# Optimization experiments

Measured on AMD Instinct MI355X. Metric: run time of the kernel, lower is better.

The kernel has to match this reference:

```python
import jax, jax.numpy as jnp
import numpy as np

N_NODES = 50000
N_EDGES = 800000
IN_CH = 64
HID = 64
N_LAYERS = 4


def setup_inputs() -> dict:
    key = jax.random.key(0)
    ks = jax.random.split(key, 10)
    x = jax.random.normal(ks[0], (N_NODES, IN_CH), dtype=jnp.float32)
    edge_index = jax.random.randint(ks[1], (2, N_EDGES), 0, N_NODES, dtype=jnp.int32)
    # SAGEConv params per layer: lin_l (applied to aggregated neighbors, with bias)
    # and lin_r (applied to root node). All layers are 64->64 so stack to [L, in, out].
    s = 1.0 / np.sqrt(IN_CH)
    Wl = jax.random.uniform(ks[2], (N_LAYERS, IN_CH, HID), jnp.float32, -s, s)
    Wr = jax.random.uniform(ks[3], (N_LAYERS, IN_CH, HID), jnp.float32, -s, s)
    b = jax.random.uniform(ks[4], (N_LAYERS, HID), jnp.float32, -s, s)
    alpha = jnp.full((N_LAYERS, HID), 0.25, dtype=jnp.float32)  # PReLU init
    return {"x": x, "edge_index": edge_index, "Wl": Wl, "Wr": Wr, "b": b, "alpha": alpha}


def _sage_layer(x, src, dst, deg_inv, Wl, Wr, b):
    # mean aggregation of source-node features at destination nodes
    agg = jax.ops.segment_sum(x[src], dst, num_segments=N_NODES)  # [N, d]
    agg = agg * deg_inv[:, None]
    return agg @ Wl + x @ Wr + b


def _prelu(x, a):
    return jnp.where(x >= 0, x, a * x)


def reference(x, edge_index, Wl, Wr, b, alpha):
    src, dst = edge_index[0], edge_index[1]
    deg = jax.ops.segment_sum(jnp.ones((N_EDGES,), jnp.float32), dst, num_segments=N_NODES)
    deg_inv = 1.0 / jnp.maximum(deg, 1.0)
    for i in range(N_LAYERS):
        x = _sage_layer(x, src, dst, deg_inv, Wl[i], Wr[i], b[i])
        x = _prelu(x, alpha[i])
    return x
```

## Files before the change

### kernel.cpp

```cpp
#include <hip/hip_runtime.h>

#define NN 50000
#define NE 800000
#define C 64
#define NL 4
#define NBK 196
#define HBLK 782

typedef __attribute__((ext_vector_type(8))) short bf16x8;
typedef __attribute__((ext_vector_type(4))) float f32x4;

__device__ __forceinline__ unsigned short f2bf(float f) {
    unsigned u = __float_as_uint(f);
    u += 0x7fffu + ((u >> 16) & 1u);
    return (unsigned short)(u >> 16);
}
__device__ __forceinline__ float4 bf4_to_f4(uint2 p) {
    float4 r;
    r.x = __uint_as_float(p.x << 16);
    r.y = __uint_as_float(p.x & 0xffff0000u);
    r.z = __uint_as_float(p.y << 16);
    r.w = __uint_as_float(p.y & 0xffff0000u);
    return r;
}

__global__ __launch_bounds__(1024) void bucket_hist_kernel(const int* __restrict__ dst,
                                                           int* __restrict__ blk_cnt,
                                                           int* __restrict__ lrank) {
    __shared__ int cnt[NBK];
    int tid = threadIdx.x;
    int blk = blockIdx.x;
    if (tid < NBK) cnt[tid] = 0;
    __syncthreads();
    int e = blk * 1024 + tid;
    if (e < NE) lrank[e] = atomicAdd(&cnt[dst[e] >> 8], 1);
    __syncthreads();
    if (tid < NBK) blk_cnt[tid * HBLK + blk] = cnt[tid];
}

__global__ __launch_bounds__(1024) void scanblk_kernel(int* __restrict__ blk_cnt,
                                                       int* __restrict__ bucket_tot) {
    __shared__ int sdata[1024];
    int b = blockIdx.x;
    int tid = threadIdx.x;
    int v = (tid < HBLK) ? blk_cnt[b * HBLK + tid] : 0;
    sdata[tid] = v;
    __syncthreads();
    for (int off = 1; off < 1024; off <<= 1) {
        int t = (tid >= off) ? sdata[tid - off] : 0;
        __syncthreads();
        sdata[tid] += t;
        __syncthreads();
    }
    if (tid < HBLK) blk_cnt[b * HBLK + tid] = sdata[tid] - v;
    if (tid == HBLK - 1) bucket_tot[b] = sdata[tid];
}

__global__ __launch_bounds__(1024) void bucket_scatter_kernel(
    const int* __restrict__ src, const int* __restrict__ dst,
    const int* __restrict__ lrank, const int* __restrict__ base2,
    const int* __restrict__ bucket_tot, int2* __restrict__ sorted) {
    __shared__ int sscan[256];
    __shared__ int sex[256];
    int tid = threadIdx.x;
    int blk = blockIdx.x;
    int v0 = 0;
    if (tid < 256) {
        v0 = (tid < NBK) ? bucket_tot[tid] : 0;
        sscan[tid] = v0;
    }
    __syncthreads();
    for (int off = 1; off < 256; off <<= 1) {
        int t = (tid < 256 && tid >= off) ? sscan[tid - off] : 0;
        __syncthreads();
        if (tid < 256) sscan[tid] += t;
        __syncthreads();
    }
    if (tid < 256) sex[tid] = sscan[tid] - v0;
    __syncthreads();

    int e = blk * 1024 + tid;
    if (e < NE) {
        int d = dst[e];
        int b = d >> 8;
        int pos = sex[b] + base2[b * HBLK + blk] + lrank[e];
        sorted[pos] = make_int2(src[e], d);
    }
}

__global__ __launch_bounds__(512) void bucket_finalize_kernel(
    const int2* __restrict__ sorted, const int* __restrict__ bucket_tot,
    int* __restrict__ row_start, int* __restrict__ deg, float* __restrict__ deg_inv,
    int* __restrict__ csr_src) {
    __shared__ int sscan[256];
    __shared__ int ldeg[256];
    __shared__ int lpre[256];
    __shared__ int lcnt[256];

    int b = blockIdx.x;
    int tid = threadIdx.x;
    int v0 = 0;
    if (tid < 256) {
        v0 = (tid < NBK) ? bucket_tot[tid] : 0;
        sscan[tid] = v0;
        ldeg[tid] = 0;
        lcnt[tid] = 0;
    }
    __syncthreads();
    for (int off = 1; off < 256; off <<= 1) {
        int t = (tid < 256 && tid >= off) ? sscan[tid - off] : 0;
        __syncthreads();
        if (tid < 256) sscan[tid] += t;
        __syncthreads();
    }
    int lo = (b == 0) ? 0 : sscan[b - 1];
    int hi = sscan[b];
    __syncthreads();

    for (int i = lo + tid; i < hi; i += 512)
        atomicAdd(&ldeg[sorted[i].y & 255], 1);
    __syncthreads();

    int dv = 0;
    if (tid < 256) {
        dv = ldeg[tid];
        lpre[tid] = dv;
    }
    __syncthreads();
    for (int off = 1; off < 256; off <<= 1) {
        int t = (tid < 256 && tid >= off) ? lpre[tid - off] : 0;
        __syncthreads();
        if (tid < 256) lpre[tid] += t;
        __syncthreads();
    }
    if (tid < 256) {
        int p = lpre[tid] - dv;
        lpre[tid] = p;
        int n = b * 256 + tid;
        if (n < NN) {
            row_start[n] = lo + p;
            deg[n] = dv;
            deg_inv[n] = 1.0f / fmaxf((float)dv, 1.0f);
        }
    }
    __syncthreads();

    for (int i = lo + tid; i < hi; i += 512) {
        int2 p = sorted[i];
        int loc = p.y & 255;
        int r = atomicAdd(&lcnt[loc], 1);
        csr_src[lo + lpre[loc] + r] = p.x;
    }
}

__global__ __launch_bounds__(512) void transform_mfma_kernel(
    const float* __restrict__ xin,
    const float* __restrict__ Wl, const float* __restrict__ Wr,
    const float* __restrict__ bias,
    unsigned short* __restrict__ y, float* __restrict__ z)
{
    __shared__ unsigned short xs[64][72];
    __shared__ unsigned short wlT[64][72];
    __shared__ unsigned short wrT[64][72];
    __shared__ unsigned short ys[64][64];
    __shared__ float zs[64][64];
    __shared__ float bs[C];

    int tid = threadIdx.x;
    int node0 = blockIdx.x * 64;

    for (int i = tid; i < C * C; i += 512) {
        int k = i >> 6, c = i & 63;
        wlT[c][k] = f2bf(Wl[i]);
        wrT[c][k] = f2bf(Wr[i]);
    }
    if (tid < C) bs[tid] = bias[tid];
    for (int i = tid; i < 64 * 16; i += 512) {
        int nl = i >> 4, c4 = i & 15;
        int n = node0 + nl;
        int nc = n < NN ? n : NN - 1;
        float4 v = ((const float4*)xin)[(size_t)nc * 16 + c4];
        xs[nl][c4 * 4 + 0] = f2bf(v.x);
        xs[nl][c4 * 4 + 1] = f2bf(v.y);
        xs[nl][c4 * 4 + 2] = f2bf(v.z);
        xs[nl][c4 * 4 + 3] = f2bf(v.w);
    }
    __syncthreads();

    int w = tid >> 6;
    int l = tid & 63;
    int mt = w >> 1;
    int half = w & 1;
    int r16 = l & 15;
    int kg = l >> 4;

    bf16x8 a0 = *(const bf16x8*)&xs[mt * 16 + r16][kg * 8];
    bf16x8 a1 = *(const bf16x8*)&xs[mt * 16 + r16][32 + kg * 8];

    f32x4 acc[4];
    #pragma unroll
    for (int nt = 0; nt < 4; nt++) {
        float bv = half ? bs[nt * 16 + r16] : 0.f;
        acc[nt] = (f32x4){bv, bv, bv, bv};
    }
    #pragma unroll
    for (int nt = 0; nt < 4; nt++) {
        const unsigned short* col = half ? &wrT[nt * 16 + r16][0] : &wlT[nt * 16 + r16][0];
        bf16x8 b0 = *(const bf16x8*)&col[kg * 8];
        bf16x8 b1 = *(const bf16x8*)&col[32 + kg * 8];
        acc[nt] = __builtin_amdgcn_mfma_f32_16x16x32_bf16(a0, b0, acc[nt], 0, 0, 0);
        acc[nt] = __builtin_amdgcn_mfma_f32_16x16x32_bf16(a1, b1, acc[nt], 0, 0, 0);
    }
    #pragma unroll
    for (int nt = 0; nt < 4; nt++) {
        #pragma unroll
        for (int j = 0; j < 4; j++) {
            int r = mt * 16 + kg * 4 + j;
            int c = nt * 16 + r16;
            if (half) zs[r][c] = acc[nt][j];
            else      ys[r][c] = f2bf(acc[nt][j]);
        }
    }
    __syncthreads();

    for (int i = tid; i < 64 * 16; i += 512) {
        int r = i >> 4, g = i & 15;
        int n = node0 + r;
        if (n < NN) {
            ((ushort4*)&y[(size_t)n * C])[g] = ((const ushort4*)&ys[r][0])[g];
            ((float4*)&z[(size_t)n * C])[g] = ((const float4*)&zs[r][0])[g];
        }
    }
}

__device__ __forceinline__ float4 gather_row(const uint2* __restrict__ yb,
                                             const int* __restrict__ cp, int d, int ql) {
    float4 acc = make_float4(0.f, 0.f, 0.f, 0.f);
    for (int t = 0; t < d; t += 8) {
        int lim = d - 1 - t;
        int j1 = min(1, lim), j2 = min(2, lim), j3 = min(3, lim);
        int j4 = min(4, lim), j5 = min(5, lim), j6 = min(6, lim), j7 = min(7, lim);
        float m1 = lim >= 1 ? 1.f : 0.f, m2 = lim >= 2 ? 1.f : 0.f;
        float m3 = lim >= 3 ? 1.f : 0.f, m4 = lim >= 4 ? 1.f : 0.f;
        float m5 = lim >= 5 ? 1.f : 0.f, m6 = lim >= 6 ? 1.f : 0.f;
        float m7 = lim >= 7 ? 1.f : 0.f;
        int s0 = cp[t];
        int s1 = cp[t + j1];
        int s2 = cp[t + j2];
        int s3 = cp[t + j3];
        int s4 = cp[t + j4];
        int s5 = cp[t + j5];
        int s6 = cp[t + j6];
        int s7 = cp[t + j7];
        uint2 p0 = yb[(size_t)s0 * 16 + ql];
        uint2 p1 = yb[(size_t)s1 * 16 + ql];
        uint2 p2 = yb[(size_t)s2 * 16 + ql];
        uint2 p3 = yb[(size_t)s3 * 16 + ql];
        uint2 p4 = yb[(size_t)s4 * 16 + ql];
        uint2 p5 = yb[(size_t)s5 * 16 + ql];
        uint2 p6 = yb[(size_t)s6 * 16 + ql];
        uint2 p7 = yb[(size_t)s7 * 16 + ql];
        float4 v0 = bf4_to_f4(p0);
        float4 v1 = bf4_to_f4(p1);
        float4 v2 = bf4_to_f4(p2);
        float4 v3 = bf4_to_f4(p3);
        float4 v4 = bf4_to_f4(p4);
        float4 v5 = bf4_to_f4(p5);
        float4 v6 = bf4_to_f4(p6);
        float4 v7 = bf4_to_f4(p7);
        acc.x += v0.x;      acc.y += v0.y;      acc.z += v0.z;      acc.w += v0.w;
        acc.x += v1.x * m1; acc.y += v1.y * m1; acc.z += v1.z * m1; acc.w += v1.w * m1;
        acc.x += v2.x * m2; acc.y += v2.y * m2; acc.z += v2.z * m2; acc.w += v2.w * m2;
        acc.x += v3.x * m3; acc.y += v3.y * m3; acc.z += v3.z * m3; acc.w += v3.w * m3;
        acc.x += v4.x * m4; acc.y += v4.y * m4; acc.z += v4.z * m4; acc.w += v4.w * m4;
        acc.x += v5.x * m5; acc.y += v5.y * m5; acc.z += v5.z * m5; acc.w += v5.w * m5;
        acc.x += v6.x * m6; acc.y += v6.y * m6; acc.z += v6.z * m6; acc.w += v6.w * m6;
        acc.x += v7.x * m7; acc.y += v7.y * m7; acc.z += v7.z * m7; acc.w += v7.w * m7;
    }
    return acc;
}

__global__ __launch_bounds__(512) void fused_gt_kernel(
    const uint2* __restrict__ yb, const float4* __restrict__ z4,
    const int* __restrict__ row_start, const int* __restrict__ deg,
    const float* __restrict__ deg_inv, const float* __restrict__ alpha,
    const int* __restrict__ csr_src,
    const float* __restrict__ Wl2, const float* __restrict__ Wr2,
    const float* __restrict__ bias2,
    unsigned short* __restrict__ yout, float* __restrict__ zout)
{
    __shared__ unsigned short wlT[64][72];
    __shared__ unsigned short wrT[64][72];
    __shared__ unsigned short xsb[32][72];
    __shared__ unsigned short ys[32][64];
    __shared__ float zs[32][64];
    __shared__ float bs2[C];

    int tid = threadIdx.x;
    for (int i = tid; i < C * C; i += 512) {
        int k = i >> 6, c = i & 63;
        wlT[c][k] = f2bf(Wl2[i]);
        wrT[c][k] = f2bf(Wr2[i]);
    }
    if (tid < C) bs2[tid] = bias2[tid];

    int nl = tid >> 4;
    int ql = tid & 15;
    int n = blockIdx.x * 32 + nl;

    float4 o = make_float4(0.f, 0.f, 0.f, 0.f);
    if (n < NN) {
        int rs = row_start[n];
        int d = deg[n];
        float4 acc = gather_row(yb, csr_src + rs, d, ql);
        float di = deg_inv[n];
        float4 zz = z4[(size_t)n * 16 + ql];
        float4 a4 = ((const float4*)alpha)[ql];
        o.x = di * acc.x + zz.x;
        o.y = di * acc.y + zz.y;
        o.z = di * acc.z + zz.z;
        o.w = di * acc.w + zz.w;
        o.x = o.x >= 0.f ? o.x : a4.x * o.x;
        o.y = o.y >= 0.f ? o.y : a4.y * o.y;
        o.z = o.z >= 0.f ? o.z : a4.z * o.z;
        o.w = o.w >= 0.f ? o.w : a4.w * o.w;
    }
    {
        ushort4 p = make_ushort4(f2bf(o.x), f2bf(o.y), f2bf(o.z), f2bf(o.w));
        *(ushort4*)&xsb[nl][ql * 4] = p;
    }
    __syncthreads();

    int w = tid >> 6;
    int l = tid & 63;
    int mt = w & 1;
    int half = (w >> 1) & 1;
    int ntg = w >> 2;
    int r16 = l & 15;
    int kg = l >> 4;

    bf16x8 a0 = *(const bf16x8*)&xsb[mt * 16 + r16][kg * 8];
    bf16x8 a1 = *(const bf16x8*)&xsb[mt * 16 + r16][32 + kg * 8];

    #pragma unroll
    for (int q = 0; q < 2; q++) {
        int nt = ntg * 2 + q;
        const unsigned short* col = half ? &wrT[nt * 16 + r16][0] : &wlT[nt * 16 + r16][0];
        bf16x8 b0 = *(const bf16x8*)&col[kg * 8];
        bf16x8 b1 = *(const bf16x8*)&col[32 + kg * 8];
        float bv = half ? bs2[nt * 16 + r16] : 0.f;
        f32x4 acc = (f32x4){bv, bv, bv, bv};
        acc = __builtin_amdgcn_mfma_f32_16x16x32_bf16(a0, b0, acc, 0, 0, 0);
        acc = __builtin_amdgcn_mfma_f32_16x16x32_bf16(a1, b1, acc, 0, 0, 0);
        #pragma unroll
        for (int j = 0; j < 4; j++) {
            int r = mt * 16 + kg * 4 + j;
            int c = nt * 16 + r16;
            if (half) zs[r][c] = acc[j];
            else      ys[r][c] = f2bf(acc[j]);
        }
    }
    __syncthreads();

    {
        int r = tid >> 4, g = tid & 15;
        int n2 = blockIdx.x * 32 + r;
        if (n2 < NN) {
            ((ushort4*)&yout[(size_t)n2 * C])[g] = ((const ushort4*)&ys[r][0])[g];
            ((float4*)&zout[(size_t)n2 * C])[g] = ((const float4*)&zs[r][0])[g];
        }
    }
}

__global__ __launch_bounds__(256) void gather_kernel(
    const uint2* __restrict__ yb, const float4* __restrict__ z4,
    const int* __restrict__ row_start, const int* __restrict__ deg,
    const float* __restrict__ deg_inv, const float* __restrict__ alpha,
    const int* __restrict__ csr_src,
    float4* __restrict__ out4)
{
    int tid = threadIdx.x;
    int n = blockIdx.x * 16 + (tid >> 4);
    int ql = tid & 15;

    int rs = row_start[n];
    int d = deg[n];
    float4 acc = gather_row(yb, csr_src + rs, d, ql);

    float di = deg_inv[n];
    float4 zz = z4[(size_t)n * 16 + ql];
    float4 a4 = ((const float4*)alpha)[ql];
    float4 o;
    o.x = di * acc.x + zz.x;
    o.y = di * acc.y + zz.y;
    o.z = di * acc.z + zz.z;
    o.w = di * acc.w + zz.w;
    o.x = o.x >= 0.f ? o.x : a4.x * o.x;
    o.y = o.y >= 0.f ? o.y : a4.y * o.y;
    o.z = o.z >= 0.f ? o.z : a4.z * o.z;
    o.w = o.w >= 0.f ? o.w : a4.w * o.w;
    out4[(size_t)n * 16 + ql] = o;
}

extern "C" void kernel_launch(void* const* d_in, const int* in_sizes, int n_in,
                              void* d_out, int out_size, void* d_ws, size_t ws_size,
                              hipStream_t stream) {
    const float* x     = (const float*)d_in[0];
    const int*   ei    = (const int*)d_in[1];
    const float* Wl    = (const float*)d_in[2];
    const float* Wr    = (const float*)d_in[3];
    const float* b     = (const float*)d_in[4];
    const float* alpha = (const float*)d_in[5];
    float* out = (float*)d_out;

    const int* src = ei;
    const int* dst = ei + NE;

    char* wsp = (char*)d_ws;
    int*  lrank        = (int*)wsp;                 wsp += (size_t)NE * 4;
    int*  blk_cnt      = (int*)wsp;                 wsp += (size_t)NBK * HBLK * 4 + 256;
    int*  bucket_tot   = (int*)wsp;                 wsp += 1024;
    int2* sorted       = (int2*)wsp;                wsp += (size_t)NE * 8;
    int*  deg          = (int*)wsp;                 wsp += (size_t)(NBK * 256) * 4;
    float* deg_inv     = (float*)wsp;               wsp += (size_t)NN * 4;
    int*  row_start    = (int*)wsp;                 wsp += (size_t)NN * 4;
    unsigned short* y0buf = (unsigned short*)wsp;   wsp += (size_t)NN * C * 2;
    unsigned short* y1buf = (unsigned short*)wsp;   wsp += (size_t)NN * C * 2;
    float* z0buf       = (float*)wsp;               wsp += (size_t)NN * C * 4;
    float* z1buf       = (float*)wsp;
    int*  csr_src      = lrank;

    bucket_hist_kernel<<<HBLK, 1024, 0, stream>>>(dst, blk_cnt, lrank);
    scanblk_kernel<<<NBK, 1024, 0, stream>>>(blk_cnt, bucket_tot);
    bucket_scatter_kernel<<<HBLK, 1024, 0, stream>>>(src, dst, lrank, blk_cnt,
                                                     bucket_tot, sorted);
    bucket_finalize_kernel<<<NBK, 512, 0, stream>>>(sorted, bucket_tot,
                                                    row_start, deg, deg_inv, csr_src);

    transform_mfma_kernel<<<(NN + 63) / 64, 512, 0, stream>>>(x, Wl, Wr, b, y0buf, z0buf);

    const int fblocks = (NN + 31) / 32;
    unsigned short* ycur = y0buf; float* zcur = z0buf;
    unsigned short* ynxt = y1buf; float* znxt = z1buf;
    for (int l = 0; l < NL - 1; l++) {
        fused_gt_kernel<<<fblocks, 512, 0, stream>>>(
            (const uint2*)ycur, (const float4*)zcur,
            row_start, deg, deg_inv, alpha + (size_t)l * C, csr_src,
            Wl + (size_t)(l + 1) * C * C, Wr + (size_t)(l + 1) * C * C,
            b + (size_t)(l + 1) * C,
            ynxt, znxt);
        unsigned short* ty = ycur; float* tz = zcur;
        ycur = ynxt; zcur = znxt;
        ynxt = ty;   znxt = tz;
    }

    gather_kernel<<<NN / 16, 256, 0, stream>>>(
        (const uint2*)ycur, (const float4*)zcur, row_start, deg,
        deg_inv, alpha + (size_t)(NL - 1) * C, csr_src, (float4*)out);
}
```

Before: 158.3 us.

## Widen gather to 8 lanes per node with 16-byte loads; pack sorted edges

The neighbor gather now gives each node 8 lanes that each load 16 bytes (8 bf16 values), where before it used 16 lanes loading 8 bytes each. This halves the number of gather load instructions and doubles node-level parallelism per block, so the fused kernel now handles 64 nodes per block and its MFMA work is split differently across warps. Separately, the sort's intermediate edge array packs the source index and the low 8 bits of the destination into a single int instead of an int2, which halves that array's traffic. The costs are more registers per thread and a packing scheme that assumes source indices fit in 24 bits.

```diff
diff --git a/kernel.cpp b/kernel.cpp
--- a/kernel.cpp
+++ b/kernel.cpp
@@ -15,14 +15,6 @@
     u += 0x7fffu + ((u >> 16) & 1u);
     return (unsigned short)(u >> 16);
 }
-__device__ __forceinline__ float4 bf4_to_f4(uint2 p) {
-    float4 r;
-    r.x = __uint_as_float(p.x << 16);
-    r.y = __uint_as_float(p.x & 0xffff0000u);
-    r.z = __uint_as_float(p.y << 16);
-    r.w = __uint_as_float(p.y & 0xffff0000u);
-    return r;
-}
 
 __global__ __launch_bounds__(1024) void bucket_hist_kernel(const int* __restrict__ dst,
                                                            int* __restrict__ blk_cnt,
@@ -59,7 +51,7 @@
 __global__ __launch_bounds__(1024) void bucket_scatter_kernel(
     const int* __restrict__ src, const int* __restrict__ dst,
     const int* __restrict__ lrank, const int* __restrict__ base2,
-    const int* __restrict__ bucket_tot, int2* __restrict__ sorted) {
+    const int* __restrict__ bucket_tot, int* __restrict__ sorted) {
     __shared__ int sscan[256];
     __shared__ int sex[256];
     int tid = threadIdx.x;
@@ -84,12 +76,12 @@
         int d = dst[e];
         int b = d >> 8;
         int pos = sex[b] + base2[b * HBLK + blk] + lrank[e];
-        sorted[pos] = make_int2(src[e], d);
+        sorted[pos] = (src[e] << 8) | (d & 255);
     }
 }
 
 __global__ __launch_bounds__(512) void bucket_finalize_kernel(
-    const int2* __restrict__ sorted, const int* __restrict__ bucket_tot,
+    const int* __restrict__ sorted, const int* __restrict__ bucket_tot,
     int* __restrict__ row_start, int* __restrict__ deg, float* __restrict__ deg_inv,
     int* __restrict__ csr_src) {
     __shared__ int sscan[256];
@@ -118,7 +110,7 @@
     __syncthreads();
 
     for (int i = lo + tid; i < hi; i += 512)
-        atomicAdd(&ldeg[sorted[i].y & 255], 1);
+        atomicAdd(&ldeg[sorted[i] & 255], 1);
     __syncthreads();
 
     int dv = 0;
@@ -146,10 +138,10 @@
     __syncthreads();
 
     for (int i = lo + tid; i < hi; i += 512) {
-        int2 p = sorted[i];
-        int loc = p.y & 255;
+        int p = sorted[i];
+        int loc = p & 255;
         int r = atomicAdd(&lcnt[loc], 1);
-        csr_src[lo + lpre[loc] + r] = p.x;
+        csr_src[lo + lpre[loc] + r] = (int)((unsigned)p >> 8);
     }
 }
 
@@ -233,9 +225,9 @@
     }
 }
 
-__device__ __forceinline__ float4 gather_row(const uint2* __restrict__ yb,
-                                             const int* __restrict__ cp, int d, int ql) {
-    float4 acc = make_float4(0.f, 0.f, 0.f, 0.f);
+__device__ __forceinline__ void gather_row8(const uint4* __restrict__ yb4,
+                                            const int* __restrict__ cp, int d, int ql,
+                                            float* __restrict__ acc) {
     for (int t = 0; t < d; t += 8) {
         int lim = d - 1 - t;
         int j1 = min(1, lim), j2 = min(2, lim), j3 = min(3, lim);
@@ -252,36 +244,31 @@
         int s5 = cp[t + j5];
         int s6 = cp[t + j6];
         int s7 = cp[t + j7];
-        uint2 p0 = yb[(size_t)s0 * 16 + ql];
-        uint2 p1 = yb[(size_t)s1 * 16 + ql];
-        uint2 p2 = yb[(size_t)s2 * 16 + ql];
-        uint2 p3 = yb[(size_t)s3 * 16 + ql];
-        uint2 p4 = yb[(size_t)s4 * 16 + ql];
-        uint2 p5 = yb[(size_t)s5 * 16 + ql];
-        uint2 p6 = yb[(size_t)s6 * 16 + ql];
-        uint2 p7 = yb[(size_t)s7 * 16 + ql];
-        float4 v0 = bf4_to_f4(p0);
-        float4 v1 = bf4_to_f4(p1);
-        float4 v2 = bf4_to_f4(p2);
-        float4 v3 = bf4_to_f4(p3);
-        float4 v4 = bf4_to_f4(p4);
-        float4 v5 = bf4_to_f4(p5);
-        float4 v6 = bf4_to_f4(p6);
-        float4 v7 = bf4_to_f4(p7);
-        acc.x += v0.x;      acc.y += v0.y;      acc.z += v0.z;      acc.w += v0.w;
-        acc.x += v1.x * m1; acc.y += v1.y * m1; acc.z += v1.z * m1; acc.w += v1.w * m1;
-        acc.x += v2.x * m2; acc.y += v2.y * m2; acc.z += v2.z * m2; acc.w += v2.w * m2;
-        acc.x += v3.x * m3; acc.y += v3.y * m3; acc.z += v3.z * m3; acc.w += v3.w * m3;
-        acc.x += v4.x * m4; acc.y += v4.y * m4; acc.z += v4.z * m4; acc.w += v4.w * m4;
-        acc.x += v5.x * m5; acc.y += v5.y * m5; acc.z += v5.z * m5; acc.w += v5.w * m5;
-        acc.x += v6.x * m6; acc.y += v6.y * m6; acc.z += v6.z * m6; acc.w += v6.w * m6;
-        acc.x += v7.x * m7; acc.y += v7.y * m7; acc.z += v7.z * m7; acc.w += v7.w * m7;
-    }
-    return acc;
+        uint4 p0 = yb4[(size_t)s0 * 8 + ql];
+        uint4 p1 = yb4[(size_t)s1 * 8 + ql];
+        uint4 p2 = yb4[(size_t)s2 * 8 + ql];
+        uint4 p3 = yb4[(size_t)s3 * 8 + ql];
+        uint4 p4 = yb4[(size_t)s4 * 8 + ql];
+        uint4 p5 = yb4[(size_t)s5 * 8 + ql];
+        uint4 p6 = yb4[(size_t)s6 * 8 + ql];
+        uint4 p7 = yb4[(size_t)s7 * 8 + ql];
+        #define ACC8(P, M) \
+            acc[0] += (M) * __uint_as_float((P).x << 16); \
+            acc[1] += (M) * __uint_as_float((P).x & 0xffff0000u); \
+            acc[2] += (M) * __uint_as_float((P).y << 16); \
+            acc[3] += (M) * __uint_as_float((P).y & 0xffff0000u); \
+            acc[4] += (M) * __uint_as_float((P).z << 16); \
+            acc[5] += (M) * __uint_as_float((P).z & 0xffff0000u); \
+            acc[6] += (M) * __uint_as_float((P).w << 16); \
+            acc[7] += (M) * __uint_as_float((P).w & 0xffff0000u);
+        ACC8(p0, 1.f) ACC8(p1, m1) ACC8(p2, m2) ACC8(p3, m3)
+        ACC8(p4, m4) ACC8(p5, m5) ACC8(p6, m6) ACC8(p7, m7)
+        #undef ACC8
+    }
 }
 
 __global__ __launch_bounds__(512) void fused_gt_kernel(
-    const uint2* __restrict__ yb, const float4* __restrict__ z4,
+    const uint4* __restrict__ yb4, const float4* __restrict__ z4,
     const int* __restrict__ row_start, const int* __restrict__ deg,
     const float* __restrict__ deg_inv, const float* __restrict__ alpha,
     const int* __restrict__ csr_src,
@@ -291,9 +278,9 @@
 {
     __shared__ unsigned short wlT[64][72];
     __shared__ unsigned short wrT[64][72];
-    __shared__ unsigned short xsb[32][72];
-    __shared__ unsigned short ys[32][64];
-    __shared__ float zs[32][64];
+    __shared__ unsigned short xsb[64][72];
+    __shared__ unsigned short ys[64][64];
+    __shared__ float zs[64][64];
     __shared__ float bs2[C];
 
     int tid = threadIdx.x;
@@ -304,38 +291,41 @@
     }
     if (tid < C) bs2[tid] = bias2[tid];
 
-    int nl = tid >> 4;
-    int ql = tid & 15;
-    int n = blockIdx.x * 32 + nl;
-
-    float4 o = make_float4(0.f, 0.f, 0.f, 0.f);
+    int nl = tid >> 3;
+    int ql = tid & 7;
+    int n = blockIdx.x * 64 + nl;
+
+    float acc[8] = {0.f, 0.f, 0.f, 0.f, 0.f, 0.f, 0.f, 0.f};
+    float o[8] = {0.f, 0.f, 0.f, 0.f, 0.f, 0.f, 0.f, 0.f};
     if (n < NN) {
         int rs = row_start[n];
         int d = deg[n];
-        float4 acc = gather_row(yb, csr_src + rs, d, ql);
+        gather_row8(yb4, csr_src + rs, d, ql, acc);
         float di = deg_inv[n];
-        float4 zz = z4[(size_t)n * 16 + ql];
-        float4 a4 = ((const float4*)alpha)[ql];
-        o.x = di * acc.x + zz.x;
-        o.y = di * acc.y + zz.y;
-        o.z = di * acc.z + zz.z;
-        o.w = di * acc.w + zz.w;
-        o.x = o.x >= 0.f ? o.x : a4.x * o.x;
-        o.y = o.y >= 0.f ? o.y : a4.y * o.y;
-        o.z = o.z >= 0.f ? o.z : a4.z * o.z;
-        o.w = o.w >= 0.f ? o.w : a4.w * o.w;
+        float4 zlo = z4[(size_t)n * 16 + ql * 2];
+        float4 zhi = z4[(size_t)n * 16 + ql * 2 + 1];
+        float4 alo = ((const float4*)alpha)[ql * 2];
+        float4 ahi = ((const float4*)alpha)[ql * 2 + 1];
+        float zv[8] = {zlo.x, zlo.y, zlo.z, zlo.w, zhi.x, zhi.y, zhi.z, zhi.w};
+        float av[8] = {alo.x, alo.y, alo.z, alo.w, ahi.x, ahi.y, ahi.z, ahi.w};
+        #pragma unroll
+        for (int j = 0; j < 8; j++) {
+            float t = di * acc[j] + zv[j];
+            o[j] = t >= 0.f ? t : av[j] * t;
+        }
     }
     {
-        ushort4 p = make_ushort4(f2bf(o.x), f2bf(o.y), f2bf(o.z), f2bf(o.w));
-        *(ushort4*)&xsb[nl][ql * 4] = p;
+        ushort4 lo = make_ushort4(f2bf(o[0]), f2bf(o[1]), f2bf(o[2]), f2bf(o[3]));
+        ushort4 hi = make_ushort4(f2bf(o[4]), f2bf(o[5]), f2bf(o[6]), f2bf(o[7]));
+        *(ushort4*)&xsb[nl][ql * 8] = lo;
+        *(ushort4*)&xsb[nl][ql * 8 + 4] = hi;
     }
     __syncthreads();
 
     int w = tid >> 6;
     int l = tid & 63;
-    int mt = w & 1;
-    int half = (w >> 1) & 1;
-    int ntg = w >> 2;
+    int mt = w >> 1;
+    int half = w & 1;
     int r16 = l & 15;
     int kg = l >> 4;
 
@@ -343,28 +333,27 @@
     bf16x8 a1 = *(const bf16x8*)&xsb[mt * 16 + r16][32 + kg * 8];
 
     #pragma unroll
-    for (int q = 0; q < 2; q++) {
-        int nt = ntg * 2 + q;
+    for (int nt = 0; nt < 4; nt++) {
         const unsigned short* col = half ? &wrT[nt * 16 + r16][0] : &wlT[nt * 16 + r16][0];
         bf16x8 b0 = *(const bf16x8*)&col[kg * 8];
         bf16x8 b1 = *(const bf16x8*)&col[32 + kg * 8];
         float bv = half ? bs2[nt * 16 + r16] : 0.f;
-        f32x4 acc = (f32x4){bv, bv, bv, bv};
-        acc = __builtin_amdgcn_mfma_f32_16x16x32_bf16(a0, b0, acc, 0, 0, 0);
-        acc = __builtin_amdgcn_mfma_f32_16x16x32_bf16(a1, b1, acc, 0, 0, 0);
+        f32x4 a4 = (f32x4){bv, bv, bv, bv};
+        a4 = __builtin_amdgcn_mfma_f32_16x16x32_bf16(a0, b0, a4, 0, 0, 0);
+        a4 = __builtin_amdgcn_mfma_f32_16x16x32_bf16(a1, b1, a4, 0, 0, 0);
         #pragma unroll
         for (int j = 0; j < 4; j++) {
             int r = mt * 16 + kg * 4 + j;
             int c = nt * 16 + r16;
-            if (half) zs[r][c] = acc[j];
-            else      ys[r][c] = f2bf(acc[j]);
-        }
-    }
-    __syncthreads();
-
-    {
-        int r = tid >> 4, g = tid & 15;
-        int n2 = blockIdx.x * 32 + r;
+            if (half) zs[r][c] = a4[j];
+            else      ys[r][c] = f2bf(a4[j]);
+        }
+    }
+    __syncthreads();
+
+    for (int i = tid; i < 64 * 16; i += 512) {
+        int r = i >> 4, g = i & 15;
+        int n2 = blockIdx.x * 64 + r;
         if (n2 < NN) {
             ((ushort4*)&yout[(size_t)n2 * C])[g] = ((const ushort4*)&ys[r][0])[g];
             ((float4*)&zout[(size_t)n2 * C])[g] = ((const float4*)&zs[r][0])[g];
@@ -373,33 +362,37 @@
 }
 
 __global__ __launch_bounds__(256) void gather_kernel(
-    const uint2* __restrict__ yb, const float4* __restrict__ z4,
+    const uint4* __restrict__ yb4, const float4* __restrict__ z4,
     const int* __restrict__ row_start, const int* __restrict__ deg,
     const float* __restrict__ deg_inv, const float* __restrict__ alpha,
     const int* __restrict__ csr_src,
     float4* __restrict__ out4)
 {
     int tid = threadIdx.x;
-    int n = blockIdx.x * 16 + (tid >> 4);
-    int ql = tid & 15;
+    int n = blockIdx.x * 32 + (tid >> 3);
+    int ql = tid & 7;
+    if (n >= NN) return;
 
     int rs = row_start[n];
     int d = deg[n];
-    float4 acc = gather_row(yb, csr_src + rs, d, ql);
+    float acc[8] = {0.f, 0.f, 0.f, 0.f, 0.f, 0.f, 0.f, 0.f};
+    gather_row8(yb4, csr_src + rs, d, ql, acc);
 
     float di = deg_inv[n];
-    float4 zz = z4[(size_t)n * 16 + ql];
-    float4 a4 = ((const float4*)alpha)[ql];
-    float4 o;
-    o.x = di * acc.x + zz.x;
-    o.y = di * acc.y + zz.y;
-    o.z = di * acc.z + zz.z;
-    o.w = di * acc.w + zz.w;
-    o.x = o.x >= 0.f ? o.x : a4.x * o.x;
-    o.y = o.y >= 0.f ? o.y : a4.y * o.y;
-    o.z = o.z >= 0.f ? o.z : a4.z * o.z;
-    o.w = o.w >= 0.f ? o.w : a4.w * o.w;
-    out4[(size_t)n * 16 + ql] = o;
+    float4 zlo = z4[(size_t)n * 16 + ql * 2];
+    float4 zhi = z4[(size_t)n * 16 + ql * 2 + 1];
+    float4 alo = ((const float4*)alpha)[ql * 2];
+    float4 ahi = ((const float4*)alpha)[ql * 2 + 1];
+    float zv[8] = {zlo.x, zlo.y, zlo.z, zlo.w, zhi.x, zhi.y, zhi.z, zhi.w};
+    float av[8] = {alo.x, alo.y, alo.z, alo.w, ahi.x, ahi.y, ahi.z, ahi.w};
+    float o[8];
+    #pragma unroll
+    for (int j = 0; j < 8; j++) {
+        float t = di * acc[j] + zv[j];
+        o[j] = t >= 0.f ? t : av[j] * t;
+    }
+    out4[(size_t)n * 16 + ql * 2]     = make_float4(o[0], o[1], o[2], o[3]);
+    out4[(size_t)n * 16 + ql * 2 + 1] = make_float4(o[4], o[5], o[6], o[7]);
 }
 
 extern "C" void kernel_launch(void* const* d_in, const int* in_sizes, int n_in,
@@ -420,7 +413,7 @@
     int*  lrank        = (int*)wsp;                 wsp += (size_t)NE * 4;
     int*  blk_cnt      = (int*)wsp;                 wsp += (size_t)NBK * HBLK * 4 + 256;
     int*  bucket_tot   = (int*)wsp;                 wsp += 1024;
-    int2* sorted       = (int2*)wsp;                wsp += (size_t)NE * 8;
+    int*  sorted       = (int*)wsp;                 wsp += (size_t)NE * 4;
     int*  deg          = (int*)wsp;                 wsp += (size_t)(NBK * 256) * 4;
     float* deg_inv     = (float*)wsp;               wsp += (size_t)NN * 4;
     int*  row_start    = (int*)wsp;                 wsp += (size_t)NN * 4;
@@ -439,12 +432,12 @@
 
     transform_mfma_kernel<<<(NN + 63) / 64, 512, 0, stream>>>(x, Wl, Wr, b, y0buf, z0buf);
 
-    const int fblocks = (NN + 31) / 32;
+    const int fblocks = (NN + 63) / 64;
     unsigned short* ycur = y0buf; float* zcur = z0buf;
     unsigned short* ynxt = y1buf; float* znxt = z1buf;
     for (int l = 0; l < NL - 1; l++) {
         fused_gt_kernel<<<fblocks, 512, 0, stream>>>(
-            (const uint2*)ycur, (const float4*)zcur,
+            (const uint4*)ycur, (const float4*)zcur,
             row_start, deg, deg_inv, alpha + (size_t)l * C, csr_src,
             Wl + (size_t)(l + 1) * C * C, Wr + (size_t)(l + 1) * C * C,
             b + (size_t)(l + 1) * C,
@@ -454,7 +447,7 @@
         ynxt = ty;   znxt = tz;
     }
 
-    gather_kernel<<<NN / 16, 256, 0, stream>>>(
-        (const uint2*)ycur, (const float4*)zcur, row_start, deg,
+    gather_kernel<<<(NN + 31) / 32, 256, 0, stream>>>(
+        (const uint4*)ycur, (const float4*)zcur, row_start, deg,
         deg_inv, alpha + (size_t)(NL - 1) * C, csr_src, (float4*)out);
 }
```

Result: slower. 168.7 us (+6.6%).
